# Optimization experiments

Measured on AMD Instinct MI355X. Metric: run time of the kernel, lower is better.

Reference implementation:

```python
import jax, jax.numpy as jnp
import numpy as np

N_NODES = 50000
N_EDGES = 800000
IN_C = 128
HID = 128
OUT_C = 64
N_LAYERS = 8
ALPHA = 0.5
THETA = 1.0


def setup_inputs() -> dict:
    key = jax.random.key(0)
    ks = jax.random.split(key, 8)
    x = jax.random.normal(ks[0], (N_NODES, IN_C), dtype=jnp.float32)
    edge_index = jax.random.randint(ks[1], (2, N_EDGES), 0, N_NODES, dtype=jnp.int32)
    edge_weight = jax.random.uniform(ks[2], (N_EDGES,), dtype=jnp.float32)
    W_in = jax.random.normal(ks[3], (IN_C, HID), dtype=jnp.float32) / np.sqrt(IN_C).astype(np.float32)
    b_in = jnp.zeros((HID,), dtype=jnp.float32)
    W_layers = jax.random.normal(ks[4], (N_LAYERS, HID, HID), dtype=jnp.float32) / np.sqrt(HID).astype(np.float32)
    W_out = jax.random.normal(ks[5], (HID, OUT_C), dtype=jnp.float32) / np.sqrt(HID).astype(np.float32)
    b_out = jnp.zeros((OUT_C,), dtype=jnp.float32)
    return {"x": x, "edge_index": edge_index, "edge_weight": edge_weight,
            "W_in": W_in, "b_in": b_in, "W_layers": W_layers,
            "W_out": W_out, "b_out": b_out}


def reference(x, edge_index, edge_weight, W_in, b_in, W_layers, W_out, b_out):
    # adj_t is pre-normalized (normalize=False); SpMM = scatter-add of gathered msgs.
    n = x.shape[0]
    src, dst = edge_index[0], edge_index[1]
    w = edge_weight[:, None]

    def spmm(feats):
        # A @ feats over edge list: gather src rows, scale, scatter-add to dst
        return jax.ops.segment_sum(feats[src] * w, dst, num_segments=n)

    # GCNConv(in->hidden): out = A (x W) + b, then ReLU
    h = jax.nn.relu(spmm(x @ W_in) + b_in)
    x0 = h

    # GCN2Conv layers (shared_weights=True, normalize=False); dropout in eval mode = identity
    for l in range(N_LAYERS):
        beta = jnp.log(THETA / (l + 1) + 1.0).astype(x.dtype)
        t = (1.0 - ALPHA) * spmm(h) + ALPHA * x0
        h = jax.nn.relu((1.0 - beta) * t + beta * (t @ W_layers[l]))

    # GCNConv(hidden->out)
    return spmm(h @ W_out) + b_out
```

## Files before the change

### kernel.cpp

```cpp
#include <hip/hip_runtime.h>
#include <math.h>

#define N_NODES 50000
#define N_EDGES 800000
#define HID 128
#define OUTC 64
#define NLAYERS 8

#define SCAN_B 64
#define SCAN_T 256
#define SCAN_C 4


__device__ __forceinline__ float bfloat_lo(unsigned int u) {
    return __int_as_float((int)(u << 16));
}
__device__ __forceinline__ float bfloat_hi(unsigned int u) {
    return __int_as_float((int)(u & 0xFFFF0000u));
}
__device__ __forceinline__ unsigned int f2bf(float f) {
    unsigned int u = (unsigned int)__float_as_int(f);
    return (u + 0x7FFFu + ((u >> 16) & 1u)) >> 16;
}
__device__ __forceinline__ unsigned int pack2bf(float a, float b) {
    return f2bf(a) | (f2bf(b) << 16);
}


__global__ void k_zero(int* __restrict__ p, int n) {
    int i = blockIdx.x * blockDim.x + threadIdx.x;
    if (i < n) p[i] = 0;
}

__global__ void k_count(const int* __restrict__ dst, int* __restrict__ deg, int E) {
    int e = blockIdx.x * blockDim.x + threadIdx.x;
    if (e < E) atomicAdd(&deg[dst[e]], 1);
}

__global__ __launch_bounds__(SCAN_T) void k_scanA(const int* __restrict__ deg, int* __restrict__ bsum) {
    __shared__ int red[SCAN_T];
    const int t = threadIdx.x, b = blockIdx.x;
    const int g = b * SCAN_T + t;
    int lo = g * SCAN_C; if (lo > N_NODES) lo = N_NODES;
    int hi = lo + SCAN_C; if (hi > N_NODES) hi = N_NODES;
    int s = 0;
    for (int i = lo; i < hi; i++) s += deg[i];
    red[t] = s;
    __syncthreads();
    for (int d = SCAN_T / 2; d > 0; d >>= 1) {
        if (t < d) red[t] += red[t + d];
        __syncthreads();
    }
    if (t == 0) bsum[b] = red[0];
}

__global__ __launch_bounds__(SCAN_T) void k_scanB(int* __restrict__ cur, int* __restrict__ off,
                                                  const int* __restrict__ bsum) {
    __shared__ int pre[SCAN_T];
    __shared__ int baseSh;
    const int t = threadIdx.x, b = blockIdx.x;
    const int g = b * SCAN_T + t;
    int lo = g * SCAN_C; if (lo > N_NODES) lo = N_NODES;
    int hi = lo + SCAN_C; if (hi > N_NODES) hi = N_NODES;
    int s = 0;
    for (int i = lo; i < hi; i++) s += cur[i];
    pre[t] = s;
    if (t == 0) {
        int acc = 0;
        for (int j = 0; j < b; j++) acc += bsum[j];
        baseSh = acc;
    }
    __syncthreads();
    for (int d = 1; d < SCAN_T; d <<= 1) {
        int v = (t >= d) ? pre[t - d] : 0;
        __syncthreads();
        pre[t] += v;
        __syncthreads();
    }
    int running = baseSh + pre[t] - s;
    for (int i = lo; i < hi; i++) {
        int d = cur[i];
        off[i] = running;
        cur[i] = running;
        running += d;
        if (i == N_NODES - 1) off[N_NODES] = running;
    }
}

__global__ void k_scatter(const int* __restrict__ src, const int* __restrict__ dst,
                          const float* __restrict__ w, int* __restrict__ cursor,
                          int2* __restrict__ ep, int E) {
    int e = blockIdx.x * blockDim.x + threadIdx.x;
    if (e < E) {
        int d = dst[e];
        int pos = atomicAdd(&cursor[d], 1);
        ep[pos] = make_int2(src[e], __float_as_int(w[e]));
    }
}

__device__ __forceinline__ void gatherB2(const int2* __restrict__ ep, int lo, int hi,
                                         const unsigned int* __restrict__ featsU, int lane,
                                         float& ax, float& ay)
{
    for (int base = lo; base < hi; base += 64) {
        const int cnt = min(hi - base, 64);
        int2 ev = make_int2(0, 0);
        if (lane < cnt) ev = ep[base + lane];
        int j = 0;
        for (; j + 8 <= cnt; j += 8) {
            int s0 = __shfl(ev.x, j + 0), s1 = __shfl(ev.x, j + 1);
            int s2 = __shfl(ev.x, j + 2), s3 = __shfl(ev.x, j + 3);
            int s4 = __shfl(ev.x, j + 4), s5 = __shfl(ev.x, j + 5);
            int s6 = __shfl(ev.x, j + 6), s7 = __shfl(ev.x, j + 7);
            float w0 = __int_as_float(__shfl(ev.y, j + 0));
            float w1 = __int_as_float(__shfl(ev.y, j + 1));
            float w2 = __int_as_float(__shfl(ev.y, j + 2));
            float w3 = __int_as_float(__shfl(ev.y, j + 3));
            float w4 = __int_as_float(__shfl(ev.y, j + 4));
            float w5 = __int_as_float(__shfl(ev.y, j + 5));
            float w6 = __int_as_float(__shfl(ev.y, j + 6));
            float w7 = __int_as_float(__shfl(ev.y, j + 7));
            unsigned int u0 = featsU[(size_t)s0 * 64 + lane];
            unsigned int u1 = featsU[(size_t)s1 * 64 + lane];
            unsigned int u2 = featsU[(size_t)s2 * 64 + lane];
            unsigned int u3 = featsU[(size_t)s3 * 64 + lane];
            unsigned int u4 = featsU[(size_t)s4 * 64 + lane];
            unsigned int u5 = featsU[(size_t)s5 * 64 + lane];
            unsigned int u6 = featsU[(size_t)s6 * 64 + lane];
            unsigned int u7 = featsU[(size_t)s7 * 64 + lane];
            ax = fmaf(w0, bfloat_lo(u0), ax); ay = fmaf(w0, bfloat_hi(u0), ay);
            ax = fmaf(w1, bfloat_lo(u1), ax); ay = fmaf(w1, bfloat_hi(u1), ay);
            ax = fmaf(w2, bfloat_lo(u2), ax); ay = fmaf(w2, bfloat_hi(u2), ay);
            ax = fmaf(w3, bfloat_lo(u3), ax); ay = fmaf(w3, bfloat_hi(u3), ay);
            ax = fmaf(w4, bfloat_lo(u4), ax); ay = fmaf(w4, bfloat_hi(u4), ay);
            ax = fmaf(w5, bfloat_lo(u5), ax); ay = fmaf(w5, bfloat_hi(u5), ay);
            ax = fmaf(w6, bfloat_lo(u6), ax); ay = fmaf(w6, bfloat_hi(u6), ay);
            ax = fmaf(w7, bfloat_lo(u7), ax); ay = fmaf(w7, bfloat_hi(u7), ay);
        }
        for (; j < cnt; j++) {
            int s = __shfl(ev.x, j);
            float w = __int_as_float(__shfl(ev.y, j));
            unsigned int u = featsU[(size_t)s * 64 + lane];
            ax = fmaf(w, bfloat_lo(u), ax); ay = fmaf(w, bfloat_hi(u), ay);
        }
    }
}

__global__ __launch_bounds__(256) void k_spmm_in(
    const int* __restrict__ off, const int2* __restrict__ ep,
    const unsigned int* __restrict__ zU, const float* __restrict__ b_in,
    unsigned int* __restrict__ hU, unsigned int* __restrict__ x0U)
{
    const int wave = threadIdx.x >> 6;
    const int lane = threadIdx.x & 63;
    const int node = blockIdx.x * 4 + wave;
    if (node >= N_NODES) return;
    const int lo = off[node], hi = off[node + 1];

    float ax = 0.f, ay = 0.f;
    gatherB2(ep, lo, hi, zU, lane, ax, ay);
    const int c = lane * 2;
    float r0 = fmaxf(ax + b_in[c], 0.f);
    float r1 = fmaxf(ay + b_in[c + 1], 0.f);
    unsigned int pk = pack2bf(r0, r1);
    hU [(size_t)node * 64 + lane] = pk;
    x0U[(size_t)node * 64 + lane] = pk;
}

__global__ __launch_bounds__(256) void k_spmm_out(
    const int* __restrict__ off, const int2* __restrict__ ep,
    const uint2* __restrict__ yU2, const float* __restrict__ b_out,
    float* __restrict__ out)
{
    const int wave = threadIdx.x >> 6;
    const int lane = threadIdx.x & 63;
    const int node = blockIdx.x * 4 + wave;
    if (node >= N_NODES) return;
    const int q = lane >> 4;
    const int s16 = lane & 15;

    float acc[4] = {0.f, 0.f, 0.f, 0.f};
    const int lo = off[node], hi = off[node + 1];
    for (int base = lo; base < hi; base += 64) {
        const int cnt = min(hi - base, 64);
        int2 ev = make_int2(0, 0);
        if (lane < cnt) ev = ep[base + lane];
        const int kmax = (cnt + 3) & ~3;
        int j = 0;
        for (; j + 8 <= kmax; j += 8) {
            int e0 = j + q, e1 = j + 4 + q;
            int s0 = __shfl(ev.x, e0), s1 = __shfl(ev.x, e1);
            float w0 = __int_as_float(__shfl(ev.y, e0));
            float w1 = __int_as_float(__shfl(ev.y, e1));
            uint2 u0 = yU2[(size_t)s0 * 16 + s16];
            uint2 u1 = yU2[(size_t)s1 * 16 + s16];
            acc[0] = fmaf(w0, bfloat_lo(u0.x), acc[0]);
            acc[1] = fmaf(w0, bfloat_hi(u0.x), acc[1]);
            acc[2] = fmaf(w0, bfloat_lo(u0.y), acc[2]);
            acc[3] = fmaf(w0, bfloat_hi(u0.y), acc[3]);
            acc[0] = fmaf(w1, bfloat_lo(u1.x), acc[0]);
            acc[1] = fmaf(w1, bfloat_hi(u1.x), acc[1]);
            acc[2] = fmaf(w1, bfloat_lo(u1.y), acc[2]);
            acc[3] = fmaf(w1, bfloat_hi(u1.y), acc[3]);
        }
        for (; j < kmax; j += 4) {
            int e = j + q;
            int s = __shfl(ev.x, e);
            float w = __int_as_float(__shfl(ev.y, e));
            uint2 u = yU2[(size_t)s * 16 + s16];
            acc[0] = fmaf(w, bfloat_lo(u.x), acc[0]);
            acc[1] = fmaf(w, bfloat_hi(u.x), acc[1]);
            acc[2] = fmaf(w, bfloat_lo(u.y), acc[2]);
            acc[3] = fmaf(w, bfloat_hi(u.y), acc[3]);
        }
    }
    #pragma unroll
    for (int i = 0; i < 4; i++) {
        acc[i] += __shfl_xor(acc[i], 16);
        acc[i] += __shfl_xor(acc[i], 32);
    }
    if (lane < 16) {
        const int c = s16 * 4;
        float4 o;
        o.x = acc[0] + b_out[c + 0];
        o.y = acc[1] + b_out[c + 1];
        o.z = acc[2] + b_out[c + 2];
        o.w = acc[3] + b_out[c + 3];
        *(float4*)(out + (size_t)node * 64 + c) = o;
    }
}

__global__ __launch_bounds__(256) void k_gemm_in(
    const float* __restrict__ A, const float* __restrict__ W,
    unsigned int* __restrict__ zU)
{
    __shared__ float As[32][128];
    const int tid = threadIdx.x;
    const int row0 = blockIdx.x * 32;
    {
        const float4* srcp = (const float4*)(A + (size_t)row0 * 128);
        float4* dl = (float4*)(&As[0][0]);
        #pragma unroll
        for (int it = 0; it < 4; it++) {
            int idx = tid + it * 256;
            int r = idx >> 5;
            float4 v = make_float4(0.f, 0.f, 0.f, 0.f);
            if (row0 + r < N_NODES) v = srcp[idx];
            dl[idx] = v;
        }
    }
    __syncthreads();

    const int rg = tid >> 5;
    const int c0 = (tid & 31) * 4;
    float acc[4][4];
    #pragma unroll
    for (int i = 0; i < 4; i++)
        #pragma unroll
        for (int j = 0; j < 4; j++) acc[i][j] = 0.f;

    #pragma unroll 4
    for (int k = 0; k < 128; k++) {
        float a0 = As[rg * 4 + 0][k], a1 = As[rg * 4 + 1][k];
        float a2 = As[rg * 4 + 2][k], a3 = As[rg * 4 + 3][k];
        float4 wv = *(const float4*)(W + (size_t)k * 128 + c0);
        float w[4] = {wv.x, wv.y, wv.z, wv.w};
        #pragma unroll
        for (int j = 0; j < 4; j++) {
            acc[0][j] = fmaf(a0, w[j], acc[0][j]);
            acc[1][j] = fmaf(a1, w[j], acc[1][j]);
            acc[2][j] = fmaf(a2, w[j], acc[2][j]);
            acc[3][j] = fmaf(a3, w[j], acc[3][j]);
        }
    }

    #pragma unroll
    for (int i = 0; i < 4; i++) {
        int r = row0 + rg * 4 + i;
        if (r < N_NODES) {
            uint2 pk = make_uint2(pack2bf(acc[i][0], acc[i][1]), pack2bf(acc[i][2], acc[i][3]));
            *(uint2*)(zU + (size_t)r * 64 + (c0 >> 1)) = pk;
        }
    }
}

__global__ __launch_bounds__(256) void k_layer(
    const int* __restrict__ off, const int2* __restrict__ ep,
    const unsigned int* __restrict__ hU, const unsigned int* __restrict__ x0U,
    const float* __restrict__ W, unsigned int* __restrict__ hOutU, float beta)
{
    __shared__ float As[32][128];
    const int tid = threadIdx.x;
    const int wave = tid >> 6, lane = tid & 63;
    const int row0 = blockIdx.x * 32;
    const int wnode0 = row0 + wave * 8;
    const int c = lane * 2;

    int offv = 0;
    if (lane < 9) {
        int nn = wnode0 + lane;
        if (nn > N_NODES) nn = N_NODES;
        offv = off[nn];
    }

    #pragma unroll 1
    for (int i = 0; i < 8; i++) {
        const int node = wnode0 + i;
        float ax = 0.f, ay = 0.f;
        if (node < N_NODES) {
            const int lo = __shfl(offv, i), hi = __shfl(offv, i + 1);
            gatherB2(ep, lo, hi, hU, lane, ax, ay);
            unsigned int xv = x0U[(size_t)node * 64 + lane];
            ax = 0.5f * ax + 0.5f * bfloat_lo(xv);
            ay = 0.5f * ay + 0.5f * bfloat_hi(xv);
        }
        *(float2*)(&As[wave * 8 + i][c]) = make_float2(ax, ay);
    }
    __syncthreads();

    const int rg = tid >> 5;
    const int c0 = (tid & 31) * 4;

    float acc[4][4];
    #pragma unroll
    for (int i = 0; i < 4; i++)
        #pragma unroll
        for (int j = 0; j < 4; j++) acc[i][j] = 0.f;

    #pragma unroll 4
    for (int k = 0; k < 128; k++) {
        float a0 = As[rg * 4 + 0][k], a1 = As[rg * 4 + 1][k];
        float a2 = As[rg * 4 + 2][k], a3 = As[rg * 4 + 3][k];
        float4 wv = *(const float4*)(W + (size_t)k * 128 + c0);
        float w[4] = {wv.x, wv.y, wv.z, wv.w};
        #pragma unroll
        for (int j = 0; j < 4; j++) {
            acc[0][j] = fmaf(a0, w[j], acc[0][j]);
            acc[1][j] = fmaf(a1, w[j], acc[1][j]);
            acc[2][j] = fmaf(a2, w[j], acc[2][j]);
            acc[3][j] = fmaf(a3, w[j], acc[3][j]);
        }
    }

    const float omb = 1.f - beta;
    #pragma unroll
    for (int i = 0; i < 4; i++) {
        int r = row0 + rg * 4 + i;
        if (r < N_NODES) {
            float v0 = fmaxf(omb * As[rg * 4 + i][c0 + 0] + beta * acc[i][0], 0.f);
            float v1 = fmaxf(omb * As[rg * 4 + i][c0 + 1] + beta * acc[i][1], 0.f);
            float v2 = fmaxf(omb * As[rg * 4 + i][c0 + 2] + beta * acc[i][2], 0.f);
            float v3 = fmaxf(omb * As[rg * 4 + i][c0 + 3] + beta * acc[i][3], 0.f);
            uint2 pk = make_uint2(pack2bf(v0, v1), pack2bf(v2, v3));
            *(uint2*)(hOutU + (size_t)r * 64 + (c0 >> 1)) = pk;
        }
    }
}

__global__ __launch_bounds__(256) void k_gemm_out(
    const unsigned int* __restrict__ hU, const float* __restrict__ W,
    unsigned int* __restrict__ yU)
{
    __shared__ float As[32][128];
    const int tid = threadIdx.x;
    const int row0 = blockIdx.x * 32;
    {
        const uint4* srcp = (const uint4*)hU;
        #pragma unroll
        for (int it = 0; it < 2; it++) {
            int idx = tid + it * 256;
            int r = idx >> 4;
            int cc = (idx & 15) * 8;
            uint4 v = make_uint4(0u, 0u, 0u, 0u);
            if (row0 + r < N_NODES) v = srcp[(size_t)(row0 + r) * 16 + (idx & 15)];
            As[r][cc + 0] = bfloat_lo(v.x); As[r][cc + 1] = bfloat_hi(v.x);
            As[r][cc + 2] = bfloat_lo(v.y); As[r][cc + 3] = bfloat_hi(v.y);
            As[r][cc + 4] = bfloat_lo(v.z); As[r][cc + 5] = bfloat_hi(v.z);
            As[r][cc + 6] = bfloat_lo(v.w); As[r][cc + 7] = bfloat_hi(v.w);
        }
    }
    __syncthreads();

    const int rg = tid >> 5;
    const int c0 = (tid & 31) * 2;
    float acc[4][2];
    #pragma unroll
    for (int i = 0; i < 4; i++) { acc[i][0] = 0.f; acc[i][1] = 0.f; }

    #pragma unroll 4
    for (int k = 0; k < 128; k++) {
        float a0 = As[rg * 4 + 0][k], a1 = As[rg * 4 + 1][k];
        float a2 = As[rg * 4 + 2][k], a3 = As[rg * 4 + 3][k];
        float2 wv = *(const float2*)(W + (size_t)k * OUTC + c0);
        acc[0][0] = fmaf(a0, wv.x, acc[0][0]); acc[0][1] = fmaf(a0, wv.y, acc[0][1]);
        acc[1][0] = fmaf(a1, wv.x, acc[1][0]); acc[1][1] = fmaf(a1, wv.y, acc[1][1]);
        acc[2][0] = fmaf(a2, wv.x, acc[2][0]); acc[2][1] = fmaf(a2, wv.y, acc[2][1]);
        acc[3][0] = fmaf(a3, wv.x, acc[3][0]); acc[3][1] = fmaf(a3, wv.y, acc[3][1]);
    }

    #pragma unroll
    for (int i = 0; i < 4; i++) {
        int r = row0 + rg * 4 + i;
        if (r < N_NODES) {
            yU[(size_t)r * 32 + (c0 >> 1)] = pack2bf(acc[i][0], acc[i][1]);
        }
    }
}


extern "C" void kernel_launch(void* const* d_in, const int* in_sizes, int n_in,
                              void* d_out, int out_size, void* d_ws, size_t ws_size,
                              hipStream_t stream)
{
    const float* x     = (const float*)d_in[0];
    const int*   ei    = (const int*)d_in[1];
    const float* ew    = (const float*)d_in[2];
    const float* W_in  = (const float*)d_in[3];
    const float* b_in  = (const float*)d_in[4];
    const float* W_lay = (const float*)d_in[5];
    const float* W_out = (const float*)d_in[6];
    const float* b_out = (const float*)d_in[7];
    float* out = (float*)d_out;

    const int* src = ei;
    const int* dst = ei + N_EDGES;

    char* p = (char*)d_ws;
    auto alloc = [&](size_t bytes) -> char* {
        char* q = p;
        p += (bytes + 255) & ~(size_t)255;
        return q;
    };
    int*          cursor = (int*)alloc((size_t)N_NODES * 4);
    int*          off    = (int*)alloc((size_t)(N_NODES + 1) * 4);
    int2*         ep     = (int2*)alloc((size_t)N_EDGES * 8);
    int*          bsum   = (int*)alloc((size_t)SCAN_B * 4);
    unsigned int* zU     = (unsigned int*)alloc((size_t)N_NODES * 64 * 4);
    unsigned int* x0U    = (unsigned int*)alloc((size_t)N_NODES * 64 * 4);
    unsigned int* hA     = (unsigned int*)alloc((size_t)N_NODES * 64 * 4);
    unsigned int* hB     = (unsigned int*)alloc((size_t)N_NODES * 64 * 4);
    unsigned int* yB     = (unsigned int*)alloc((size_t)N_NODES * 32 * 4);

    k_zero<<<(N_NODES + 255) / 256, 256, 0, stream>>>(cursor, N_NODES);
    k_count<<<(N_EDGES + 255) / 256, 256, 0, stream>>>(dst, cursor, N_EDGES);
    k_scanA<<<SCAN_B, SCAN_T, 0, stream>>>(cursor, bsum);
    k_scanB<<<SCAN_B, SCAN_T, 0, stream>>>(cursor, off, bsum);
    k_scatter<<<(N_EDGES + 255) / 256, 256, 0, stream>>>(src, dst, ew, cursor, ep, N_EDGES);

    const int gemmGrid  = (N_NODES + 31) / 32;
    const int spmmGrid  = (N_NODES + 3) / 4;

    k_gemm_in<<<gemmGrid, 256, 0, stream>>>(x, W_in, zU);
    k_spmm_in<<<spmmGrid, 256, 0, stream>>>(off, ep, zU, b_in, hA, x0U);

    unsigned int* hin = hA;
    unsigned int* hout = hB;
    for (int l = 0; l < NLAYERS; l++) {
        float beta = logf(1.0f / (float)(l + 1) + 1.0f);
        k_layer<<<gemmGrid, 256, 0, stream>>>(off, ep, hin, x0U,
                                              W_lay + (size_t)l * HID * HID, hout, beta);
        unsigned int* tmp = hin; hin = hout; hout = tmp;
    }

    k_gemm_out<<<gemmGrid, 256, 0, stream>>>(hin, W_out, yB);
    k_spmm_out<<<spmmGrid, 256, 0, stream>>>(off, ep, (const uint2*)yB, b_out, out);
}
```

Measured before the change: 748.4 us.

## Gather two nodes per iteration and prefetch next pair's edge lists

The per-node SpMM gather in the fused GCN2 layer kernel now handles two destination nodes at a time. It interleaves 16 independent row loads per inner step to raise memory-level parallelism, and it prefetches the next pair's edge (index, weight) entries into registers ahead of use. Nodes with more than 64 edges fall back to the old gatherB2 path. The cost is higher register pressure, which may reduce occupancy, plus wasted loads when the two nodes have unequal degree. Padding lanes use index 0 with weight 0, so the result stays correct.

After: 714.9 us. 1.05x faster.

```diff
diff --git a/kernel.cpp b/kernel.cpp
--- a/kernel.cpp
+++ b/kernel.cpp
@@ -303,18 +303,110 @@
         offv = off[nn];
     }
 
+    int loA = __shfl(offv, 0), hiA = __shfl(offv, 1), hiB = __shfl(offv, 2);
+    int2 evA = make_int2(0, 0), evB = make_int2(0, 0);
+    if (lane < min(hiA - loA, 64)) evA = ep[loA + lane];
+    if (lane < min(hiB - hiA, 64)) evB = ep[hiA + lane];
+
     #pragma unroll 1
-    for (int i = 0; i < 8; i++) {
-        const int node = wnode0 + i;
-        float ax = 0.f, ay = 0.f;
-        if (node < N_NODES) {
-            const int lo = __shfl(offv, i), hi = __shfl(offv, i + 1);
-            gatherB2(ep, lo, hi, hU, lane, ax, ay);
-            unsigned int xv = x0U[(size_t)node * 64 + lane];
-            ax = 0.5f * ax + 0.5f * bfloat_lo(xv);
-            ay = 0.5f * ay + 0.5f * bfloat_hi(xv);
-        }
-        *(float2*)(&As[wave * 8 + i][c]) = make_float2(ax, ay);
+    for (int p = 0; p < 4; p++) {
+        const int nodeA = wnode0 + 2 * p, nodeB = nodeA + 1;
+        const int dA = hiA - loA, dB = hiB - hiA;
+        const int loB = hiA;
+        const bool vA = nodeA < N_NODES, vB = nodeB < N_NODES;
+
+        int nloA = 0, nhiA = 0, nhiB = 0;
+        int2 nevA = make_int2(0, 0), nevB = make_int2(0, 0);
+        if (p < 3) {
+            nloA = __shfl(offv, 2 * p + 2);
+            nhiA = __shfl(offv, 2 * p + 3);
+            nhiB = __shfl(offv, 2 * p + 4);
+            if (lane < min(nhiA - nloA, 64)) nevA = ep[nloA + lane];
+            if (lane < min(nhiB - nhiA, 64)) nevB = ep[nhiA + lane];
+        }
+
+        unsigned int xvA = 0, xvB = 0;
+        if (vA) xvA = x0U[(size_t)nodeA * 64 + lane];
+        if (vB) xvB = x0U[(size_t)nodeB * 64 + lane];
+
+        float axA = 0.f, ayA = 0.f, axB = 0.f, ayB = 0.f;
+        if (dA <= 64 && dB <= 64) {
+            const int kmax = max(dA, dB);
+            for (int j = 0; j < kmax; j += 8) {
+                int a0 = __shfl(evA.x, j + 0), a1 = __shfl(evA.x, j + 1);
+                int a2 = __shfl(evA.x, j + 2), a3 = __shfl(evA.x, j + 3);
+                int a4 = __shfl(evA.x, j + 4), a5 = __shfl(evA.x, j + 5);
+                int a6 = __shfl(evA.x, j + 6), a7 = __shfl(evA.x, j + 7);
+                int b0 = __shfl(evB.x, j + 0), b1 = __shfl(evB.x, j + 1);
+                int b2 = __shfl(evB.x, j + 2), b3 = __shfl(evB.x, j + 3);
+                int b4 = __shfl(evB.x, j + 4), b5 = __shfl(evB.x, j + 5);
+                int b6 = __shfl(evB.x, j + 6), b7 = __shfl(evB.x, j + 7);
+                unsigned int uA0 = hU[(size_t)a0 * 64 + lane];
+                unsigned int uA1 = hU[(size_t)a1 * 64 + lane];
+                unsigned int uA2 = hU[(size_t)a2 * 64 + lane];
+                unsigned int uA3 = hU[(size_t)a3 * 64 + lane];
+                unsigned int uA4 = hU[(size_t)a4 * 64 + lane];
+                unsigned int uA5 = hU[(size_t)a5 * 64 + lane];
+                unsigned int uA6 = hU[(size_t)a6 * 64 + lane];
+                unsigned int uA7 = hU[(size_t)a7 * 64 + lane];
+                unsigned int uB0 = hU[(size_t)b0 * 64 + lane];
+                unsigned int uB1 = hU[(size_t)b1 * 64 + lane];
+                unsigned int uB2 = hU[(size_t)b2 * 64 + lane];
+                unsigned int uB3 = hU[(size_t)b3 * 64 + lane];
+                unsigned int uB4 = hU[(size_t)b4 * 64 + lane];
+                unsigned int uB5 = hU[(size_t)b5 * 64 + lane];
+                unsigned int uB6 = hU[(size_t)b6 * 64 + lane];
+                unsigned int uB7 = hU[(size_t)b7 * 64 + lane];
+                float wA0 = __int_as_float(__shfl(evA.y, j + 0));
+                float wA1 = __int_as_float(__shfl(evA.y, j + 1));
+                float wA2 = __int_as_float(__shfl(evA.y, j + 2));
+                float wA3 = __int_as_float(__shfl(evA.y, j + 3));
+                float wA4 = __int_as_float(__shfl(evA.y, j + 4));
+                float wA5 = __int_as_float(__shfl(evA.y, j + 5));
+                float wA6 = __int_as_float(__shfl(evA.y, j + 6));
+                float wA7 = __int_as_float(__shfl(evA.y, j + 7));
+                float wB0 = __int_as_float(__shfl(evB.y, j + 0));
+                float wB1 = __int_as_float(__shfl(evB.y, j + 1));
+                float wB2 = __int_as_float(__shfl(evB.y, j + 2));
+                float wB3 = __int_as_float(__shfl(evB.y, j + 3));
+                float wB4 = __int_as_float(__shfl(evB.y, j + 4));
+                float wB5 = __int_as_float(__shfl(evB.y, j + 5));
+                float wB6 = __int_as_float(__shfl(evB.y, j + 6));
+                float wB7 = __int_as_float(__shfl(evB.y, j + 7));
+                axA = fmaf(wA0, bfloat_lo(uA0), axA); ayA = fmaf(wA0, bfloat_hi(uA0), ayA);
+                axB = fmaf(wB0, bfloat_lo(uB0), axB); ayB = fmaf(wB0, bfloat_hi(uB0), ayB);
+                axA = fmaf(wA1, bfloat_lo(uA1), axA); ayA = fmaf(wA1, bfloat_hi(uA1), ayA);
+                axB = fmaf(wB1, bfloat_lo(uB1), axB); ayB = fmaf(wB1, bfloat_hi(uB1), ayB);
+                axA = fmaf(wA2, bfloat_lo(uA2), axA); ayA = fmaf(wA2, bfloat_hi(uA2), ayA);
+                axB = fmaf(wB2, bfloat_lo(uB2), axB); ayB = fmaf(wB2, bfloat_hi(uB2), ayB);
+                axA = fmaf(wA3, bfloat_lo(uA3), axA); ayA = fmaf(wA3, bfloat_hi(uA3), ayA);
+                axB = fmaf(wB3, bfloat_lo(uB3), axB); ayB = fmaf(wB3, bfloat_hi(uB3), ayB);
+                axA = fmaf(wA4, bfloat_lo(uA4), axA); ayA = fmaf(wA4, bfloat_hi(uA4), ayA);
+                axB = fmaf(wB4, bfloat_lo(uB4), axB); ayB = fmaf(wB4, bfloat_hi(uB4), ayB);
+                axA = fmaf(wA5, bfloat_lo(uA5), axA); ayA = fmaf(wA5, bfloat_hi(uA5), ayA);
+                axB = fmaf(wB5, bfloat_lo(uB5), axB); ayB = fmaf(wB5, bfloat_hi(uB5), ayB);
+                axA = fmaf(wA6, bfloat_lo(uA6), axA); ayA = fmaf(wA6, bfloat_hi(uA6), ayA);
+                axB = fmaf(wB6, bfloat_lo(uB6), axB); ayB = fmaf(wB6, bfloat_hi(uB6), ayB);
+                axA = fmaf(wA7, bfloat_lo(uA7), axA); ayA = fmaf(wA7, bfloat_hi(uA7), ayA);
+                axB = fmaf(wB7, bfloat_lo(uB7), axB); ayB = fmaf(wB7, bfloat_hi(uB7), ayB);
+            }
+        } else {
+            gatherB2(ep, loA, hiA, hU, lane, axA, ayA);
+            gatherB2(ep, loB, hiB, hU, lane, axB, ayB);
+        }
+
+        if (vA) {
+            axA = 0.5f * axA + 0.5f * bfloat_lo(xvA);
+            ayA = 0.5f * ayA + 0.5f * bfloat_hi(xvA);
+        } else { axA = 0.f; ayA = 0.f; }
+        if (vB) {
+            axB = 0.5f * axB + 0.5f * bfloat_lo(xvB);
+            ayB = 0.5f * ayB + 0.5f * bfloat_hi(xvB);
+        } else { axB = 0.f; ayB = 0.f; }
+        *(float2*)(&As[wave * 8 + 2 * p + 0][c]) = make_float2(axA, ayA);
+        *(float2*)(&As[wave * 8 + 2 * p + 1][c]) = make_float2(axB, ayB);
+
+        loA = nloA; hiA = nhiA; hiB = nhiB; evA = nevA; evB = nevB;
     }
     __syncthreads();
 
```
